# Performance work log

Hardware: AMD Instinct MI355X
Metric: run time of the kernel (lower is better)

## Reference

```python
import jax, jax.numpy as jnp
import numpy as np


def setup_inputs() -> dict:
    key = jax.random.key(0)
    kx, ka, kw, kk = jax.random.split(key, 4)
    N, F, D, K = 4096, 256, 128, 2
    X = jax.random.normal(kx, (N, F), dtype=jnp.float32)
    # K+1 dense adjacency/distance matrices; uniform(0,1) keeps degrees positive
    adj = jax.random.uniform(ka, (K + 1, N, N), dtype=jnp.float32)
    W_emb = jax.random.normal(kw, (F, D), dtype=jnp.float32) / np.float32(np.sqrt(F))
    kernels = jax.random.normal(kk, (K + 1, F, D), dtype=jnp.float32) / np.float32(np.sqrt(F))
    alpha = jnp.float32(0.1)
    return {"X": X, "adj": adj, "W_emb": W_emb, "kernels": kernels, "alpha": alpha}


def reference(X, adj, W_emb, kernels, alpha):
    # X: [N,F], adj: [K+1,N,N], W_emb: [F,D], kernels: [K+1,F,D], alpha: scalar
    E = X @ W_emb                                # [N,D] learned embeddings
    low_rank = alpha * (E @ E.T)                 # [N,N] rank-D correction, shared across hops
    XK = jnp.einsum('nf,kfd->knd', X, kernels)   # [K+1,N,D] hop-wise kernel projections
    out = jnp.zeros((X.shape[0], kernels.shape[-1]), dtype=X.dtype)
    for hop in range(adj.shape[0]):              # small fixed K+1 loop
        A_hat = adj[hop] + low_rank              # [N,N]
        d = jax.lax.rsqrt(jnp.sum(A_hat, axis=1))  # deg^{-1/2}; diag-matmul == broadcast scale
        A_norm = d[:, None] * A_hat * d[None, :]  # D^{-1/2} A_hat D^{-1/2}
        out = out + A_norm @ XK[hop]
    return jax.nn.relu(out)
```

## Files before the change

### kernel.cpp

```cpp
#include <hip/hip_runtime.h>
#include <hip/hip_bf16.h>

#define Nn 4096
#define Fdim 256
#define Ddim 128
#define NH 3

typedef __bf16 bf16x8 __attribute__((ext_vector_type(8)));
typedef float f32x4 __attribute__((ext_vector_type(4)));
typedef unsigned short ushort8v __attribute__((ext_vector_type(8)));
typedef unsigned short ushort4v __attribute__((ext_vector_type(4)));

#define MFMA(a, b, c) __builtin_amdgcn_mfma_f32_16x16x32_bf16((a), (b), (c), 0, 0, 0)

__device__ __forceinline__ float bf2f(unsigned short u) {
    union { unsigned int i; float f; } cv;
    cv.i = ((unsigned int)u) << 16;
    return cv.f;
}
__device__ __forceinline__ unsigned short f2bf(float f) {
    union { __bf16 b; unsigned short u; } cv;
    cv.b = (__bf16)f;
    return cv.u;
}
__device__ __forceinline__ bf16x8 cvt8(const float* p, float s) {
    const float4 lo = *(const float4*)p;
    const float4 hi = *(const float4*)(p + 4);
    bf16x8 r;
    r[0] = (__bf16)(lo.x * s); r[1] = (__bf16)(lo.y * s);
    r[2] = (__bf16)(lo.z * s); r[3] = (__bf16)(lo.w * s);
    r[4] = (__bf16)(hi.x * s); r[5] = (__bf16)(hi.y * s);
    r[6] = (__bf16)(hi.z * s); r[7] = (__bf16)(hi.w * s);
    return r;
}

__global__ void kprobe(const unsigned short* __restrict__ X, float* __restrict__ mode,
                       float* __restrict__ s) {
    int t = threadIdx.x;
    s[t] = 0.f;
    s[t + 64] = 0.f;
    int wild = 0;
    for (int i = t; i < 2048; i += 64) {
        unsigned short u = X[i];
        int e = (u >> 7) & 0xFF;
        if (e >= 132) wild = 1;
    }
    unsigned long long m = __ballot(wild != 0);
    if (t == 0) mode[0] = (__popcll(m) > 4) ? 0.0f : 1.0f;
}

__global__ void k0_wt(const void* __restrict__ W_emb, const void* __restrict__ kernels,
                      unsigned short* __restrict__ WT, const float* __restrict__ mode) {
    bool isbf = mode[0] > 0.5f;
    int b = blockIdx.x, nt = b >> 1, fh = b & 1;
    __shared__ unsigned short T[128][136];
    int t = threadIdx.x;
    int d4 = t & 31, fr = t >> 5;
    if (isbf) {
        const unsigned short* Wsrc = (nt == 0) ? (const unsigned short*)W_emb
                                               : ((const unsigned short*)kernels + (size_t)(nt - 1) * Fdim * Ddim);
        for (int p = 0; p < 16; ++p) {
            int fl = fr + 8 * p;
            int f = fh * 128 + fl;
            ushort4v v = *(const ushort4v*)(Wsrc + (size_t)f * Ddim + 4 * d4);
            T[4 * d4 + 0][fl] = v[0]; T[4 * d4 + 1][fl] = v[1];
            T[4 * d4 + 2][fl] = v[2]; T[4 * d4 + 3][fl] = v[3];
        }
    } else {
        const float* Wsrc = (nt == 0) ? (const float*)W_emb
                                      : ((const float*)kernels + (size_t)(nt - 1) * Fdim * Ddim);
        for (int p = 0; p < 16; ++p) {
            int fl = fr + 8 * p;
            int f = fh * 128 + fl;
            float4 v = *(const float4*)(Wsrc + (size_t)f * Ddim + 4 * d4);
            T[4 * d4 + 0][fl] = f2bf(v.x); T[4 * d4 + 1][fl] = f2bf(v.y);
            T[4 * d4 + 2][fl] = f2bf(v.z); T[4 * d4 + 3][fl] = f2bf(v.w);
        }
    }
    __syncthreads();
    int f4 = t & 31, dr = t >> 5;
    for (int p = 0; p < 16; ++p) {
        int dd = dr + 8 * p;
        ushort4v w;
        w[0] = T[dd][4 * f4 + 0]; w[1] = T[dd][4 * f4 + 1];
        w[2] = T[dd][4 * f4 + 2]; w[3] = T[dd][4 * f4 + 3];
        *(ushort4v*)(WT + (size_t)nt * Ddim * Fdim + (size_t)dd * Fdim + fh * 128 + 4 * f4) = w;
    }
}

__global__ void k1_proj(const void* __restrict__ Xv, const unsigned short* __restrict__ WT,
                        float* __restrict__ E, float* __restrict__ XK,
                        const float* __restrict__ mode) {
    bool isbf = mode[0] > 0.5f;
    int mt = blockIdx.x >> 2, nt = blockIdx.x & 3;
    int t = threadIdx.x, wid = t >> 6, lane = t & 63, l15 = lane & 15, q = lane >> 4;
    int m0 = mt * 16;
    const unsigned short* BT = WT + (size_t)nt * Ddim * Fdim;
    const unsigned short* b0p = BT + (size_t)(wid * 32 + l15) * Fdim;
    const unsigned short* b1p = b0p + 16 * Fdim;
    f32x4 acc0 = {0.f, 0.f, 0.f, 0.f}, acc1 = {0.f, 0.f, 0.f, 0.f};
    if (isbf) {
        const unsigned short* Arow = (const unsigned short*)Xv + (size_t)(m0 + l15) * Fdim;
#pragma unroll
        for (int ks = 0; ks < 8; ++ks) {
            int kk = ks * 32 + q * 8;
            bf16x8 a = *(const bf16x8*)(Arow + kk);
            bf16x8 b0 = *(const bf16x8*)(b0p + kk);
            bf16x8 b1 = *(const bf16x8*)(b1p + kk);
            acc0 = MFMA(a, b0, acc0);
            acc1 = MFMA(a, b1, acc1);
        }
    } else {
        const float* Arow = (const float*)Xv + (size_t)(m0 + l15) * Fdim;
#pragma unroll
        for (int ks = 0; ks < 8; ++ks) {
            int kk = ks * 32 + q * 8;
            bf16x8 a = cvt8(Arow + kk, 1.0f);
            bf16x8 b0 = *(const bf16x8*)(b0p + kk);
            bf16x8 b1 = *(const bf16x8*)(b1p + kk);
            acc0 = MFMA(a, b0, acc0);
            acc1 = MFMA(a, b1, acc1);
        }
    }
    float* dst = (nt == 0) ? E : (XK + (size_t)(nt - 1) * Nn * Ddim);
#pragma unroll
    for (int r = 0; r < 4; ++r) {
        int ml = q * 4 + r;
        dst[(size_t)(m0 + ml) * Ddim + wid * 32 + l15] = acc0[r];
        dst[(size_t)(m0 + ml) * Ddim + wid * 32 + 16 + l15] = acc1[r];
    }
}

__global__ void k2_rowsum(const void* __restrict__ adjv, float* __restrict__ rowsum,
                          const float* __restrict__ mode) {
    bool isbf = mode[0] > 0.5f;
    int t = threadIdx.x, w = t >> 6, lane = t & 63;
    int r = blockIdx.x * 4 + w;
    float sum = 0.f;
    if (isbf) {
        const unsigned short* rp = (const unsigned short*)adjv + (size_t)r * Nn;
#pragma unroll
        for (int it = 0; it < 8; ++it) {
            ushort8v v = *(const ushort8v*)(rp + (it * 64 + lane) * 8);
            sum += bf2f(v[0]) + bf2f(v[1]) + bf2f(v[2]) + bf2f(v[3]) +
                   bf2f(v[4]) + bf2f(v[5]) + bf2f(v[6]) + bf2f(v[7]);
        }
    } else {
        const float4* rp = (const float4*)((const float*)adjv + (size_t)r * Nn);
#pragma unroll
        for (int it = 0; it < 16; ++it) {
            float4 v = rp[it * 64 + lane];
            sum += v.x + v.y + v.z + v.w;
        }
    }
#pragma unroll
    for (int off = 32; off > 0; off >>= 1) sum += __shfl_down(sum, off, 64);
    if (lane == 0) rowsum[r] = sum;
}

__global__ void k3_colsum(const float* __restrict__ E, float* __restrict__ s) {
    int c = threadIdx.x;
    int r0 = blockIdx.x * 16;
    float p = 0.f;
#pragma unroll
    for (int r = 0; r < 16; ++r)
        p += E[(size_t)(r0 + r) * Ddim + c];
    atomicAdd(&s[c], p);
}

__global__ void k4_dgen(const float* __restrict__ E, const float* __restrict__ rowsum,
                        const float* __restrict__ s, const void* __restrict__ alphap,
                        float* __restrict__ dbuf, const float* __restrict__ mode) {
    bool isbf = mode[0] > 0.5f;
    __shared__ float ss[128];
    int t = threadIdx.x;
    if (t < 128) ss[t] = s[t];
    __syncthreads();
    int wid = t >> 6, lane = t & 63;
    int node = blockIdx.x * 32 + wid * 8 + (lane >> 3);
    int sub = lane & 7;
    const float4* er = (const float4*)(E + (size_t)node * Ddim + sub * 16);
    float acc = 0.f;
#pragma unroll
    for (int k = 0; k < 4; ++k) {
        float4 v = er[k];
        int c = sub * 16 + 4 * k;
        acc += v.x * ss[c] + v.y * ss[c + 1] + v.z * ss[c + 2] + v.w * ss[c + 3];
    }
#pragma unroll
    for (int off = 1; off < 8; off <<= 1) acc += __shfl_xor(acc, off, 64);
    if (sub == 0) {
        float a = isbf ? bf2f(((const unsigned short*)alphap)[0]) : ((const float*)alphap)[0];
#pragma unroll
        for (int h = 0; h < NH; ++h)
            dbuf[h * Nn + node] = rsqrtf(rowsum[h * Nn + node] + a * acc);
    }
}

__global__ void k5_transpose(const float* __restrict__ XK, const float* __restrict__ E,
                             const float* __restrict__ dbuf, unsigned short* __restrict__ Yp,
                             unsigned short* __restrict__ ET) {
    __shared__ unsigned short T[128][72];
    __shared__ float sl[64];
    int b = blockIdx.x, t = threadIdx.x;
    bool isET = (b >= 192);
    int h = 0, jt;
    const float* src;
    if (!isET) { h = b >> 6; jt = b & 63; src = XK + (size_t)h * Nn * Ddim; }
    else { jt = b - 192; src = E; }
    if (t < 64) sl[t] = isET ? 1.0f : dbuf[h * Nn + jt * 64 + t];
    __syncthreads();
    int d4 = t & 31, jr = t >> 5;
    for (int p = 0; p < 8; ++p) {
        int j = jr + 8 * p;
        float4 v = *(const float4*)(src + (size_t)(jt * 64 + j) * Ddim + 4 * d4);
        float sc = sl[j];
        T[4 * d4 + 0][j] = f2bf(v.x * sc); T[4 * d4 + 1][j] = f2bf(v.y * sc);
        T[4 * d4 + 2][j] = f2bf(v.z * sc); T[4 * d4 + 3][j] = f2bf(v.w * sc);
    }
    __syncthreads();
    int jj4 = t & 15, nr = t >> 4;
    unsigned short* dst = isET ? ET : (Yp + (size_t)h * Ddim * Nn);
    for (int p = 0; p < 8; ++p) {
        int n = nr + 16 * p;
        ushort4v w;
        w[0] = T[n][4 * jj4 + 0]; w[1] = T[n][4 * jj4 + 1];
        w[2] = T[n][4 * jj4 + 2]; w[3] = T[n][4 * jj4 + 3];
        int j = jt * 64 + 4 * jj4;
        *(ushort4v*)(dst + (size_t)n * Nn + j) = w;
    }
}

__global__ void k6_mgen(const unsigned short* __restrict__ ET,
                        const unsigned short* __restrict__ Yp, float* __restrict__ Mpart) {
    int b = blockIdx.x;
    int kc = b / 24, rem = b % 24, h = rem >> 3, mtm = rem & 7;
    int t = threadIdx.x, wid = t >> 6, lane = t & 63, l15 = lane & 15, q = lane >> 4;
    int m0 = mtm * 16;
    const unsigned short* Ar = ET + (size_t)(m0 + l15) * Nn + kc * 512;
    const unsigned short* Yph = Yp + (size_t)h * Ddim * Nn;
    const unsigned short* bb = Yph + (size_t)(wid * 32 + l15) * Nn + kc * 512 + q * 8;
    f32x4 acc0 = {0.f, 0.f, 0.f, 0.f}, acc1 = {0.f, 0.f, 0.f, 0.f};
#pragma unroll 4
    for (int ks = 0; ks < 16; ++ks) {
        bf16x8 a = *(const bf16x8*)(Ar + ks * 32 + q * 8);
        bf16x8 b0 = *(const bf16x8*)(bb + ks * 32);
        bf16x8 b1 = *(const bf16x8*)(bb + (size_t)16 * Nn + ks * 32);
        acc0 = MFMA(a, b0, acc0);
        acc1 = MFMA(a, b1, acc1);
    }
    float* out = Mpart + (size_t)kc * (NH * Ddim * Ddim) + (size_t)h * (Ddim * Ddim);
#pragma unroll
    for (int r = 0; r < 4; ++r) {
        int ml = q * 4 + r;
        out[(m0 + ml) * Ddim + wid * 32 + l15] = acc0[r];
        out[(m0 + ml) * Ddim + wid * 32 + 16 + l15] = acc1[r];
    }
}

__global__ void k6b_mred(const float* __restrict__ Mpart, unsigned short* __restrict__ MT) {
    int idx = blockIdx.x * 256 + threadIdx.x;
    int d2 = idx / 384, kcol = idx % 384;
    int h = kcol >> 7, d1 = kcol & 127;
    float sum = 0.f;
#pragma unroll
    for (int kc = 0; kc < 8; ++kc)
        sum += Mpart[(size_t)kc * (NH * Ddim * Ddim) + h * (Ddim * Ddim) + d1 * Ddim + d2];
    MT[idx] = f2bf(sum);
}

__global__ void k8_lgen(const float* __restrict__ E, const float* __restrict__ dbuf,
                        const void* __restrict__ alphap, const unsigned short* __restrict__ MT,
                        float* __restrict__ L, const float* __restrict__ mode) {
    bool isbf = mode[0] > 0.5f;
    int mt = blockIdx.x;
    int t = threadIdx.x, wid = t >> 6, lane = t & 63, l15 = lane & 15, q = lane >> 4;
    int m0 = mt * 16, m = m0 + l15;
    float a = isbf ? bf2f(((const unsigned short*)alphap)[0]) : ((const float*)alphap)[0];
    float dv[NH];
#pragma unroll
    for (int h = 0; h < NH; ++h) dv[h] = a * dbuf[h * Nn + m];
    const float* Er = E + (size_t)m * Ddim;
    const unsigned short* b0p = MT + (size_t)(wid * 32 + l15) * 384;
    const unsigned short* b1p = b0p + 16 * 384;
    f32x4 acc0 = {0.f, 0.f, 0.f, 0.f}, acc1 = {0.f, 0.f, 0.f, 0.f};
#pragma unroll
    for (int ks = 0; ks < 12; ++ks) {
        int kk = ks * 32;
        int h = kk >> 7;
        int kloc = (kk & 127) + q * 8;
        bf16x8 aa = cvt8(Er + kloc, dv[h]);
        bf16x8 b0 = *(const bf16x8*)(b0p + kk + q * 8);
        bf16x8 b1 = *(const bf16x8*)(b1p + kk + q * 8);
        acc0 = MFMA(aa, b0, acc0);
        acc1 = MFMA(aa, b1, acc1);
    }
#pragma unroll
    for (int r = 0; r < 4; ++r) {
        int ml = q * 4 + r;
        L[(size_t)(m0 + ml) * Ddim + wid * 32 + l15] = acc0[r];
        L[(size_t)(m0 + ml) * Ddim + wid * 32 + 16 + l15] = acc1[r];
    }
}

__global__ void kzero(float* __restrict__ P) {
    size_t base = ((size_t)blockIdx.x * 256 + threadIdx.x) * 4;
    float4 z; z.x = 0.f; z.y = 0.f; z.z = 0.f; z.w = 0.f;
    *(float4*)(P + base) = z;
}

__global__ void __launch_bounds__(512, 2) k7_fused(const void* __restrict__ adjv,
        const unsigned short* __restrict__ Yp, const float* __restrict__ dbuf,
        float* __restrict__ P, const float* __restrict__ mode) {
    bool isbf = mode[0] > 0.5f;
    __shared__ unsigned short lds[2][6][4096];
    __shared__ float dsh[NH][128];
    int b = blockIdx.x;
    int mt = b >> 3, kc = b & 7;
    int m0 = mt * 128;
    int kbase = kc * 512;
    int t = threadIdx.x;
    if (t < 384) { int h = t >> 7, m = t & 127; dsh[h][m] = dbuf[h * Nn + m0 + m]; }

    int sr = t >> 2, ss = t & 3;
    int sw = ss ^ ((sr >> 2) & 3);
    const float* aBaseF = (const float*)adjv + (size_t)(m0 + sr) * Nn + kbase + 8 * sw;
    const unsigned short* aBaseH = (const unsigned short*)adjv + (size_t)(m0 + sr) * Nn + kbase + 8 * sw;
    const unsigned short* bBase = Yp + (size_t)sr * Nn + kbase + 8 * sw;

    int wid = t >> 6, lane = t & 63, l15 = lane & 15, q = lane >> 4;
    int wm = wid >> 1, wn = wid & 1;
    f32x4 acc[NH][2][4] = {};

    float4 ApF[NH][2];
    ushort8v ApH[NH];
    ushort8v Bpr[NH];

    auto stage_load = [&](int c) {
        int ko = c * 32;
        if (isbf) {
#pragma unroll
            for (int h = 0; h < NH; ++h)
                ApH[h] = *(const ushort8v*)(aBaseH + (size_t)h * Nn * Nn + ko);
        } else {
#pragma unroll
            for (int h = 0; h < NH; ++h) {
                ApF[h][0] = *(const float4*)(aBaseF + (size_t)h * Nn * Nn + ko);
                ApF[h][1] = *(const float4*)(aBaseF + (size_t)h * Nn * Nn + ko + 4);
            }
        }
#pragma unroll
        for (int h = 0; h < NH; ++h)
            Bpr[h] = *(const ushort8v*)(bBase + (size_t)h * Ddim * Nn + ko);
    };
    auto stage_write = [&](int buf) {
#pragma unroll
        for (int h = 0; h < NH; ++h) {
            ushort8v w;
            if (isbf) w = ApH[h];
            else {
                w[0] = f2bf(ApF[h][0].x); w[1] = f2bf(ApF[h][0].y);
                w[2] = f2bf(ApF[h][0].z); w[3] = f2bf(ApF[h][0].w);
                w[4] = f2bf(ApF[h][1].x); w[5] = f2bf(ApF[h][1].y);
                w[6] = f2bf(ApF[h][1].z); w[7] = f2bf(ApF[h][1].w);
            }
            *(ushort8v*)&lds[buf][h][t * 8] = w;
            *(ushort8v*)&lds[buf][3 + h][t * 8] = Bpr[h];
        }
    };
    auto compute = [&](int buf) {
#pragma unroll
        for (int h = 0; h < NH; ++h) {
            bf16x8 af[2], bfr[4];
#pragma unroll
            for (int i = 0; i < 2; ++i) {
                int m = wm * 32 + i * 16 + l15;
                af[i] = *(const bf16x8*)&lds[buf][h][m * 32 + (q ^ ((m >> 2) & 3)) * 8];
            }
#pragma unroll
            for (int j = 0; j < 4; ++j) {
                int n = wn * 64 + j * 16 + l15;
                bfr[j] = *(const bf16x8*)&lds[buf][3 + h][n * 32 + (q ^ ((n >> 2) & 3)) * 8];
            }
#pragma unroll
            for (int i = 0; i < 2; ++i)
#pragma unroll
                for (int j = 0; j < 4; ++j)
                    acc[h][i][j] = MFMA(af[i], bfr[j], acc[h][i][j]);
        }
    };

    stage_load(0);
    stage_write(0);
    __syncthreads();
#pragma unroll 2
    for (int c = 0; c < 16; ++c) {
        if (c < 15) stage_load(c + 1);
        compute(c & 1);
        if (c < 15) {
            stage_write((c + 1) & 1);
            __syncthreads();
        }
    }

#pragma unroll
    for (int i = 0; i < 2; ++i) {
#pragma unroll
        for (int r = 0; r < 4; ++r) {
            int row = wm * 32 + i * 16 + q * 4 + r;
            float d0 = dsh[0][row], d1 = dsh[1][row], d2 = dsh[2][row];
            float* pr = P + (size_t)(m0 + row) * Ddim + wn * 64 + l15;
#pragma unroll
            for (int j = 0; j < 4; ++j) {
                float v = d0 * acc[0][i][j][r] + d1 * acc[1][i][j][r] + d2 * acc[2][i][j][r];
                atomicAdd(pr + j * 16, v);
            }
        }
    }
}

__global__ void k9_combine(const float* __restrict__ P, const float* __restrict__ L,
                           void* __restrict__ outv, const float* __restrict__ mode) {
    bool isbf = mode[0] > 0.5f;
    size_t base = ((size_t)blockIdx.x * 256 + threadIdx.x) * 4;
    float4 v0 = *(const float4*)(P + base);
    float4 vl = *(const float4*)(L + base);
    float r0 = v0.x + vl.x;
    float r1 = v0.y + vl.y;
    float r2 = v0.z + vl.z;
    float r3 = v0.w + vl.w;
    r0 = r0 > 0.f ? r0 : 0.f;
    r1 = r1 > 0.f ? r1 : 0.f;
    r2 = r2 > 0.f ? r2 : 0.f;
    r3 = r3 > 0.f ? r3 : 0.f;
    if (isbf) {
        ushort4v w;
        w[0] = f2bf(r0); w[1] = f2bf(r1); w[2] = f2bf(r2); w[3] = f2bf(r3);
        *(ushort4v*)((unsigned short*)outv + base) = w;
    } else {
        float4 w; w.x = r0; w.y = r1; w.z = r2; w.w = r3;
        *(float4*)((float*)outv + base) = w;
    }
}

extern "C" void kernel_launch(void* const* d_in, const int* in_sizes, int n_in,
                              void* d_out, int out_size, void* d_ws, size_t ws_size,
                              hipStream_t stream) {
    const void* X = d_in[0];
    const void* adj = d_in[1];
    const void* W_emb = d_in[2];
    const void* kernels = d_in[3];
    const void* alphap = d_in[4];

    float* E = (float*)d_ws;
    float* XK = E + 524288;
    float* rowsum = XK + 1572864;
    float* s = rowsum + 12288;
    float* dbuf = s + 128;
    float* Mpart = dbuf + 12288;
    float* L = Mpart + 393216;
    unsigned short* WT = (unsigned short*)(L + 524288);
    unsigned short* ET = WT + 131072;
    unsigned short* Yp = ET + 524288;
    unsigned short* MT = Yp + 1572864;
    float* modef = (float*)(MT + 49152);
    float* P = XK;

    kprobe<<<1, 64, 0, stream>>>((const unsigned short*)X, modef, s);
    k2_rowsum<<<3072, 256, 0, stream>>>(adj, rowsum, modef);
    k0_wt<<<8, 256, 0, stream>>>(W_emb, kernels, WT, modef);
    k1_proj<<<1024, 256, 0, stream>>>(X, WT, E, XK, modef);
    k3_colsum<<<256, 128, 0, stream>>>(E, s);
    k4_dgen<<<128, 256, 0, stream>>>(E, rowsum, s, alphap, dbuf, modef);
    k5_transpose<<<256, 256, 0, stream>>>(XK, E, dbuf, Yp, ET);
    kzero<<<512, 256, 0, stream>>>(P);
    k6_mgen<<<192, 256, 0, stream>>>(ET, Yp, Mpart);
    k6b_mred<<<192, 256, 0, stream>>>(Mpart, MT);
    k8_lgen<<<256, 256, 0, stream>>>(E, dbuf, alphap, MT, L, modef);
    k7_fused<<<256, 512, 0, stream>>>(adj, Yp, dbuf, P, modef);
    k9_combine<<<512, 256, 0, stream>>>(P, L, d_out, modef);
}
```

Before: 398.9 us.

## Pre-convert adjacency to bf16 in rowsum pass and replace atomics with split-K partials

The rowsum kernel, which already reads the fp32 adjacency, now also writes a bf16 copy to workspace. The fused main kernel then streams half as many bytes and skips the per-element conversion. The main kernel also writes per-K-chunk partial outputs with plain stores instead of atomicAdd, and the combine kernel sums the 8 partials, so the zeroing kernel is dropped. In exchange, a ~100MB bf16 copy of the adjacency is written and read back, plus 8 partial buffers, which adds memory traffic.

```diff
diff --git a/kernel.cpp b/kernel.cpp
--- a/kernel.cpp
+++ b/kernel.cpp
@@ -132,7 +132,7 @@
 }
 
 __global__ void k2_rowsum(const void* __restrict__ adjv, float* __restrict__ rowsum,
-                          const float* __restrict__ mode) {
+                          unsigned short* __restrict__ adjB, const float* __restrict__ mode) {
     bool isbf = mode[0] > 0.5f;
     int t = threadIdx.x, w = t >> 6, lane = t & 63;
     int r = blockIdx.x * 4 + w;
@@ -147,10 +147,14 @@
         }
     } else {
         const float4* rp = (const float4*)((const float*)adjv + (size_t)r * Nn);
+        unsigned short* wp = adjB + (size_t)r * Nn;
 #pragma unroll
         for (int it = 0; it < 16; ++it) {
             float4 v = rp[it * 64 + lane];
             sum += v.x + v.y + v.z + v.w;
+            ushort4v o;
+            o[0] = f2bf(v.x); o[1] = f2bf(v.y); o[2] = f2bf(v.z); o[3] = f2bf(v.w);
+            *(ushort4v*)(wp + (it * 64 + lane) * 4) = o;
         }
     }
 #pragma unroll
@@ -303,15 +307,10 @@
     }
 }
 
-__global__ void kzero(float* __restrict__ P) {
-    size_t base = ((size_t)blockIdx.x * 256 + threadIdx.x) * 4;
-    float4 z; z.x = 0.f; z.y = 0.f; z.z = 0.f; z.w = 0.f;
-    *(float4*)(P + base) = z;
-}
-
 __global__ void __launch_bounds__(512, 2) k7_fused(const void* __restrict__ adjv,
-        const unsigned short* __restrict__ Yp, const float* __restrict__ dbuf,
-        float* __restrict__ P, const float* __restrict__ mode) {
+        const unsigned short* __restrict__ adjB, const unsigned short* __restrict__ Yp,
+        const float* __restrict__ dbuf, float* __restrict__ Pp,
+        const float* __restrict__ mode) {
     bool isbf = mode[0] > 0.5f;
     __shared__ unsigned short lds[2][6][4096];
     __shared__ float dsh[NH][128];
@@ -322,49 +321,32 @@
     int t = threadIdx.x;
     if (t < 384) { int h = t >> 7, m = t & 127; dsh[h][m] = dbuf[h * Nn + m0 + m]; }
 
+    const unsigned short* adjS = isbf ? (const unsigned short*)adjv : adjB;
+
     int sr = t >> 2, ss = t & 3;
     int sw = ss ^ ((sr >> 2) & 3);
-    const float* aBaseF = (const float*)adjv + (size_t)(m0 + sr) * Nn + kbase + 8 * sw;
-    const unsigned short* aBaseH = (const unsigned short*)adjv + (size_t)(m0 + sr) * Nn + kbase + 8 * sw;
+    const unsigned short* aBase = adjS + (size_t)(m0 + sr) * Nn + kbase + 8 * sw;
     const unsigned short* bBase = Yp + (size_t)sr * Nn + kbase + 8 * sw;
 
     int wid = t >> 6, lane = t & 63, l15 = lane & 15, q = lane >> 4;
     int wm = wid >> 1, wn = wid & 1;
     f32x4 acc[NH][2][4] = {};
 
-    float4 ApF[NH][2];
-    ushort8v ApH[NH];
+    ushort8v Apr[NH];
     ushort8v Bpr[NH];
 
     auto stage_load = [&](int c) {
         int ko = c * 32;
-        if (isbf) {
-#pragma unroll
-            for (int h = 0; h < NH; ++h)
-                ApH[h] = *(const ushort8v*)(aBaseH + (size_t)h * Nn * Nn + ko);
-        } else {
-#pragma unroll
-            for (int h = 0; h < NH; ++h) {
-                ApF[h][0] = *(const float4*)(aBaseF + (size_t)h * Nn * Nn + ko);
-                ApF[h][1] = *(const float4*)(aBaseF + (size_t)h * Nn * Nn + ko + 4);
-            }
-        }
-#pragma unroll
-        for (int h = 0; h < NH; ++h)
+#pragma unroll
+        for (int h = 0; h < NH; ++h) {
+            Apr[h] = *(const ushort8v*)(aBase + (size_t)h * Nn * Nn + ko);
             Bpr[h] = *(const ushort8v*)(bBase + (size_t)h * Ddim * Nn + ko);
+        }
     };
     auto stage_write = [&](int buf) {
 #pragma unroll
         for (int h = 0; h < NH; ++h) {
-            ushort8v w;
-            if (isbf) w = ApH[h];
-            else {
-                w[0] = f2bf(ApF[h][0].x); w[1] = f2bf(ApF[h][0].y);
-                w[2] = f2bf(ApF[h][0].z); w[3] = f2bf(ApF[h][0].w);
-                w[4] = f2bf(ApF[h][1].x); w[5] = f2bf(ApF[h][1].y);
-                w[6] = f2bf(ApF[h][1].z); w[7] = f2bf(ApF[h][1].w);
-            }
-            *(ushort8v*)&lds[buf][h][t * 8] = w;
+            *(ushort8v*)&lds[buf][h][t * 8] = Apr[h];
             *(ushort8v*)&lds[buf][3 + h][t * 8] = Bpr[h];
         }
     };
@@ -403,32 +385,34 @@
         }
     }
 
+    float* Pk = Pp + (size_t)kc * (Nn * Ddim);
 #pragma unroll
     for (int i = 0; i < 2; ++i) {
 #pragma unroll
         for (int r = 0; r < 4; ++r) {
             int row = wm * 32 + i * 16 + q * 4 + r;
             float d0 = dsh[0][row], d1 = dsh[1][row], d2 = dsh[2][row];
-            float* pr = P + (size_t)(m0 + row) * Ddim + wn * 64 + l15;
+            float* pr = Pk + (size_t)(m0 + row) * Ddim + wn * 64 + l15;
 #pragma unroll
             for (int j = 0; j < 4; ++j) {
                 float v = d0 * acc[0][i][j][r] + d1 * acc[1][i][j][r] + d2 * acc[2][i][j][r];
-                atomicAdd(pr + j * 16, v);
+                pr[j * 16] = v;
             }
         }
     }
 }
 
-__global__ void k9_combine(const float* __restrict__ P, const float* __restrict__ L,
+__global__ void k9_combine(const float* __restrict__ Pp, const float* __restrict__ L,
                            void* __restrict__ outv, const float* __restrict__ mode) {
     bool isbf = mode[0] > 0.5f;
     size_t base = ((size_t)blockIdx.x * 256 + threadIdx.x) * 4;
-    float4 v0 = *(const float4*)(P + base);
-    float4 vl = *(const float4*)(L + base);
-    float r0 = v0.x + vl.x;
-    float r1 = v0.y + vl.y;
-    float r2 = v0.z + vl.z;
-    float r3 = v0.w + vl.w;
+    float4 a = *(const float4*)(L + base);
+    float r0 = a.x, r1 = a.y, r2 = a.z, r3 = a.w;
+#pragma unroll
+    for (int kc = 0; kc < 8; ++kc) {
+        float4 v = *(const float4*)(Pp + (size_t)kc * (Nn * Ddim) + base);
+        r0 += v.x; r1 += v.y; r2 += v.z; r3 += v.w;
+    }
     r0 = r0 > 0.f ? r0 : 0.f;
     r1 = r1 > 0.f ? r1 : 0.f;
     r2 = r2 > 0.f ? r2 : 0.f;
@@ -459,24 +443,24 @@
     float* dbuf = s + 128;
     float* Mpart = dbuf + 12288;
     float* L = Mpart + 393216;
-    unsigned short* WT = (unsigned short*)(L + 524288);
+    float* Pp = L + 524288;
+    unsigned short* WT = (unsigned short*)(Pp + 8 * 524288);
     unsigned short* ET = WT + 131072;
     unsigned short* Yp = ET + 524288;
     unsigned short* MT = Yp + 1572864;
-    float* modef = (float*)(MT + 49152);
-    float* P = XK;
+    unsigned short* adjB = MT + 49152;
+    float* modef = (float*)(adjB + (size_t)NH * Nn * Nn);
 
     kprobe<<<1, 64, 0, stream>>>((const unsigned short*)X, modef, s);
-    k2_rowsum<<<3072, 256, 0, stream>>>(adj, rowsum, modef);
+    k2_rowsum<<<3072, 256, 0, stream>>>(adj, rowsum, adjB, modef);
     k0_wt<<<8, 256, 0, stream>>>(W_emb, kernels, WT, modef);
     k1_proj<<<1024, 256, 0, stream>>>(X, WT, E, XK, modef);
     k3_colsum<<<256, 128, 0, stream>>>(E, s);
     k4_dgen<<<128, 256, 0, stream>>>(E, rowsum, s, alphap, dbuf, modef);
     k5_transpose<<<256, 256, 0, stream>>>(XK, E, dbuf, Yp, ET);
-    kzero<<<512, 256, 0, stream>>>(P);
     k6_mgen<<<192, 256, 0, stream>>>(ET, Yp, Mpart);
     k6b_mred<<<192, 256, 0, stream>>>(Mpart, MT);
     k8_lgen<<<256, 256, 0, stream>>>(E, dbuf, alphap, MT, L, modef);
-    k7_fused<<<256, 512, 0, stream>>>(adj, Yp, dbuf, P, modef);
-    k9_combine<<<512, 256, 0, stream>>>(P, L, d_out, modef);
-}
+    k7_fused<<<256, 512, 0, stream>>>(adj, adjB, Yp, dbuf, Pp, modef);
+    k9_combine<<<512, 256, 0, stream>>>(Pp, L, d_out, modef);
+}
```

Result: slower. 410.5 us (+2.9%).

## Fuse column sums into projection and replace split-K atomics with partial buffers

Applied to the files above, without the earlier changes.

Computes the embedding column sums inside the projection kernel via wave shuffles and atomics, removing the separate colsum kernel. The split-K fused adjacency kernel now writes plain stores into eight per-chunk partial buffers instead of atomically adding into a zeroed accumulator, so the zeroing kernel is dropped and the combine kernel sums the eight partials. Launch bounds for the main kernel change to one block per SM hint, and kernel launch order is shuffled. This trades atomic contention for extra memory traffic (8x partial writes and reads, about 16 MB each way) and more workspace.

```diff
diff --git a/kernel.cpp b/kernel.cpp
--- a/kernel.cpp
+++ b/kernel.cpp
@@ -89,7 +89,7 @@
 }
 
 __global__ void k1_proj(const void* __restrict__ Xv, const unsigned short* __restrict__ WT,
-                        float* __restrict__ E, float* __restrict__ XK,
+                        float* __restrict__ E, float* __restrict__ XK, float* __restrict__ s,
                         const float* __restrict__ mode) {
     bool isbf = mode[0] > 0.5f;
     int mt = blockIdx.x >> 2, nt = blockIdx.x & 3;
@@ -129,6 +129,16 @@
         dst[(size_t)(m0 + ml) * Ddim + wid * 32 + l15] = acc0[r];
         dst[(size_t)(m0 + ml) * Ddim + wid * 32 + 16 + l15] = acc1[r];
     }
+    if (nt == 0) {
+        float c0 = acc0[0] + acc0[1] + acc0[2] + acc0[3];
+        float c1 = acc1[0] + acc1[1] + acc1[2] + acc1[3];
+        c0 += __shfl_xor(c0, 16, 64); c0 += __shfl_xor(c0, 32, 64);
+        c1 += __shfl_xor(c1, 16, 64); c1 += __shfl_xor(c1, 32, 64);
+        if (q == 0) {
+            atomicAdd(&s[wid * 32 + l15], c0);
+            atomicAdd(&s[wid * 32 + 16 + l15], c1);
+        }
+    }
 }
 
 __global__ void k2_rowsum(const void* __restrict__ adjv, float* __restrict__ rowsum,
@@ -156,16 +166,6 @@
 #pragma unroll
     for (int off = 32; off > 0; off >>= 1) sum += __shfl_down(sum, off, 64);
     if (lane == 0) rowsum[r] = sum;
-}
-
-__global__ void k3_colsum(const float* __restrict__ E, float* __restrict__ s) {
-    int c = threadIdx.x;
-    int r0 = blockIdx.x * 16;
-    float p = 0.f;
-#pragma unroll
-    for (int r = 0; r < 16; ++r)
-        p += E[(size_t)(r0 + r) * Ddim + c];
-    atomicAdd(&s[c], p);
 }
 
 __global__ void k4_dgen(const float* __restrict__ E, const float* __restrict__ rowsum,
@@ -303,15 +303,9 @@
     }
 }
 
-__global__ void kzero(float* __restrict__ P) {
-    size_t base = ((size_t)blockIdx.x * 256 + threadIdx.x) * 4;
-    float4 z; z.x = 0.f; z.y = 0.f; z.z = 0.f; z.w = 0.f;
-    *(float4*)(P + base) = z;
-}
-
-__global__ void __launch_bounds__(512, 2) k7_fused(const void* __restrict__ adjv,
+__global__ void __launch_bounds__(512, 1) k7_fused(const void* __restrict__ adjv,
         const unsigned short* __restrict__ Yp, const float* __restrict__ dbuf,
-        float* __restrict__ P, const float* __restrict__ mode) {
+        float* __restrict__ Pp, const float* __restrict__ mode) {
     bool isbf = mode[0] > 0.5f;
     __shared__ unsigned short lds[2][6][4096];
     __shared__ float dsh[NH][128];
@@ -403,32 +397,34 @@
         }
     }
 
+    float* Pk = Pp + (size_t)kc * (Nn * Ddim);
 #pragma unroll
     for (int i = 0; i < 2; ++i) {
 #pragma unroll
         for (int r = 0; r < 4; ++r) {
             int row = wm * 32 + i * 16 + q * 4 + r;
             float d0 = dsh[0][row], d1 = dsh[1][row], d2 = dsh[2][row];
-            float* pr = P + (size_t)(m0 + row) * Ddim + wn * 64 + l15;
+            float* pr = Pk + (size_t)(m0 + row) * Ddim + wn * 64 + l15;
 #pragma unroll
             for (int j = 0; j < 4; ++j) {
                 float v = d0 * acc[0][i][j][r] + d1 * acc[1][i][j][r] + d2 * acc[2][i][j][r];
-                atomicAdd(pr + j * 16, v);
+                pr[j * 16] = v;
             }
         }
     }
 }
 
-__global__ void k9_combine(const float* __restrict__ P, const float* __restrict__ L,
+__global__ void k9_combine(const float* __restrict__ Pp, const float* __restrict__ L,
                            void* __restrict__ outv, const float* __restrict__ mode) {
     bool isbf = mode[0] > 0.5f;
     size_t base = ((size_t)blockIdx.x * 256 + threadIdx.x) * 4;
-    float4 v0 = *(const float4*)(P + base);
-    float4 vl = *(const float4*)(L + base);
-    float r0 = v0.x + vl.x;
-    float r1 = v0.y + vl.y;
-    float r2 = v0.z + vl.z;
-    float r3 = v0.w + vl.w;
+    float4 a = *(const float4*)(L + base);
+    float r0 = a.x, r1 = a.y, r2 = a.z, r3 = a.w;
+#pragma unroll
+    for (int kc = 0; kc < 8; ++kc) {
+        float4 v = *(const float4*)(Pp + (size_t)kc * (Nn * Ddim) + base);
+        r0 += v.x; r1 += v.y; r2 += v.z; r3 += v.w;
+    }
     r0 = r0 > 0.f ? r0 : 0.f;
     r1 = r1 > 0.f ? r1 : 0.f;
     r2 = r2 > 0.f ? r2 : 0.f;
@@ -459,24 +455,22 @@
     float* dbuf = s + 128;
     float* Mpart = dbuf + 12288;
     float* L = Mpart + 393216;
-    unsigned short* WT = (unsigned short*)(L + 524288);
+    float* Pp = L + 524288;
+    unsigned short* WT = (unsigned short*)(Pp + 8 * 524288);
     unsigned short* ET = WT + 131072;
     unsigned short* Yp = ET + 524288;
     unsigned short* MT = Yp + 1572864;
     float* modef = (float*)(MT + 49152);
-    float* P = XK;
 
     kprobe<<<1, 64, 0, stream>>>((const unsigned short*)X, modef, s);
+    k0_wt<<<8, 256, 0, stream>>>(W_emb, kernels, WT, modef);
+    k1_proj<<<1024, 256, 0, stream>>>(X, WT, E, XK, s, modef);
     k2_rowsum<<<3072, 256, 0, stream>>>(adj, rowsum, modef);
-    k0_wt<<<8, 256, 0, stream>>>(W_emb, kernels, WT, modef);
-    k1_proj<<<1024, 256, 0, stream>>>(X, WT, E, XK, modef);
-    k3_colsum<<<256, 128, 0, stream>>>(E, s);
     k4_dgen<<<128, 256, 0, stream>>>(E, rowsum, s, alphap, dbuf, modef);
     k5_transpose<<<256, 256, 0, stream>>>(XK, E, dbuf, Yp, ET);
-    kzero<<<512, 256, 0, stream>>>(P);
     k6_mgen<<<192, 256, 0, stream>>>(ET, Yp, Mpart);
     k6b_mred<<<192, 256, 0, stream>>>(Mpart, MT);
     k8_lgen<<<256, 256, 0, stream>>>(E, dbuf, alphap, MT, L, modef);
-    k7_fused<<<256, 512, 0, stream>>>(adj, Yp, dbuf, P, modef);
-    k9_combine<<<512, 256, 0, stream>>>(P, L, d_out, modef);
-}
+    k7_fused<<<256, 512, 0, stream>>>(adj, Yp, dbuf, Pp, modef);
+    k9_combine<<<512, 256, 0, stream>>>(Pp, L, d_out, modef);
+}
```

After: 388.1 us. -2.7%, faster.
